# Performance work log

Hardware: AMD Instinct MI355X
Metric: run time of the kernel (lower is better)

Reference implementation:

```python
import jax, jax.numpy as jnp
import numpy as np

D_MODEL = 1024
N_HEADS = 16
D_HEAD = D_MODEL // N_HEADS


def setup_inputs() -> dict:
    key = jax.random.key(0)
    k_x, k_qkv, k_proj = jax.random.split(key, 3)
    x = jax.random.normal(k_x, (4, 2048, D_MODEL), dtype=jnp.float32)
    # nn.Linear(d_model, 3*d_model, bias=False): weight shape [3*d_model, d_model]
    scale = 1.0 / np.sqrt(D_MODEL)
    W_qkv = jax.random.uniform(k_qkv, (3 * D_MODEL, D_MODEL), dtype=jnp.float32, minval=-scale, maxval=scale)
    W_proj = jax.random.uniform(k_proj, (D_MODEL, D_MODEL), dtype=jnp.float32, minval=-scale, maxval=scale)
    return {"x": x, "W_qkv": W_qkv, "W_proj": W_proj}


def reference(x, W_qkv, W_proj):
    B, T, C = x.shape
    qkv = jnp.einsum('btc,fc->btf', x, W_qkv)  # [B,T,3C]
    q, k, v = jnp.split(qkv, 3, axis=-1)
    # [B,T,H,Dh] -> [B,H,T,Dh]
    q = q.reshape(B, T, N_HEADS, D_HEAD).transpose(0, 2, 1, 3)
    k = k.reshape(B, T, N_HEADS, D_HEAD).transpose(0, 2, 1, 3)
    v = v.reshape(B, T, N_HEADS, D_HEAD).transpose(0, 2, 1, 3)
    att = jnp.einsum('bhqd,bhkd->bhqk', q, k) / jnp.sqrt(jnp.float32(D_HEAD))
    att = jax.nn.softmax(att, axis=-1)
    y = jnp.einsum('bhqk,bhkd->bhqd', att, v)
    y = y.transpose(0, 2, 1, 3).reshape(B, T, C)
    return jnp.einsum('btc,oc->bto', y, W_proj)
```

## Files before the change

### kernel.cpp

```cpp
#include <hip/hip_runtime.h>
#include <stdint.h>
#include <stddef.h>

#define SEQ   2048
#define NH    16
#define DH    64
#define DM    1024
#define NTOK  8192

typedef unsigned short u16;
typedef unsigned int u32;
typedef short bf16x8 __attribute__((ext_vector_type(8)));
typedef float f32x4  __attribute__((ext_vector_type(4)));
typedef unsigned short u16x4 __attribute__((ext_vector_type(4)));
typedef unsigned short u16x8 __attribute__((ext_vector_type(8)));

#define QSCALE 0.18033688011112042f

#define WAIT_VM12 0x0F7C
#define WAIT_VM2  0x0F72
#define WAIT_VM0  0x0F70

__device__ __forceinline__ u16 f2bf(float f) {
  union { float f; unsigned u; } v; v.f = f;
  return (u16)((v.u + 0x7FFFu + ((v.u >> 16) & 1u)) >> 16);
}

__device__ __forceinline__ void gload_lds16(const void* g, void* l) {
  __builtin_amdgcn_global_load_lds(
      (const __attribute__((address_space(1))) void*)g,
      (__attribute__((address_space(3))) void*)l, 16, 0, 0);
}

__global__ __launch_bounds__(256) void cast_kernel(const float* __restrict__ src,
                                                   u16* __restrict__ dst, int n4) {
  int i = blockIdx.x * 256 + threadIdx.x;
  if (i < n4) {
    const float4 f = ((const float4*)src)[i];
    u16x4 o;
    o.x = f2bf(f.x); o.y = f2bf(f.y); o.z = f2bf(f.z); o.w = f2bf(f.w);
    ((u16x4*)dst)[i] = o;
  }
}

__global__ __launch_bounds__(256) void pack_b(const float* __restrict__ W,
                                              u16* __restrict__ Bp, int NS) {
  const int chunk = blockIdx.x * 256 + threadIdx.x;
  const int lane = chunk & 63, blk = chunk >> 6;
  const int c = blk / NS, s = blk % NS;
  const int n = s * 16 + (lane & 15);
  const int k0 = c * 32 + (lane >> 4) * 8;
  const float4 f0 = *(const float4*)&W[(size_t)n * DM + k0];
  const float4 f1 = *(const float4*)&W[(size_t)n * DM + k0 + 4];
  u16x8 o;
  o[0] = f2bf(f0.x); o[1] = f2bf(f0.y); o[2] = f2bf(f0.z); o[3] = f2bf(f0.w);
  o[4] = f2bf(f1.x); o[5] = f2bf(f1.y); o[6] = f2bf(f1.z); o[7] = f2bf(f1.w);
  *(u16x8*)&Bp[(size_t)chunk * 8] = o;
}

template <int EPI>
__global__ __launch_bounds__(256) void gemm_flat(
    const u16* __restrict__ A, const u16* __restrict__ Bp, int NS, int N_,
    u16* __restrict__ Qo, u16* __restrict__ Ko, u16* __restrict__ Vto,
    float* __restrict__ Co) {
  __shared__ __align__(16) u16 sA[2][128 * 64];
  const int tid = threadIdx.x;
  const int wave = tid >> 6, lane = tid & 63;
  const int l16 = lane & 15, quad = lane >> 4;
  const int sw = l16 & 7;
  const int wm = (wave >> 1) * 64, wn = (wave & 1) * 64;
  const int nbx = (int)gridDim.x;
  const int id = (int)(blockIdx.y * nbx + blockIdx.x);
  const int cpx = (int)(gridDim.x * gridDim.y) >> 3;
  const int wid = (id & 7) * cpx + (id >> 3);
  const int row0 = (wid / nbx) * 128, col0 = (wid % nbx) * 128;
  const int ck0 = ((quad ^ sw) << 3);
  const int ck1 = (((quad + 4) ^ sw) << 3);
  const int scol = (col0 + wn) >> 4;
  const u16* bpw = Bp + (size_t)lane * 8;

  f32x4 acc[4][4];
  for (int a = 0; a < 4; ++a)
    for (int b = 0; b < 4; ++b) acc[a][b] = (f32x4){0.f, 0.f, 0.f, 0.f};

  bf16x8 bfr[2][2][4];

  for (int j = 0; j < 4; ++j) {
    const int li = j * 256 + tid;
    const int r = li >> 3;
    const int cs = (((li & 7) ^ (r & 7)) << 3);
    gload_lds16(A + (size_t)(row0 + r) * DM + cs, (char*)sA[0] + li * 16);
  }
  for (int kk = 0; kk < 2; ++kk) {
    const u16* bb = bpw + ((size_t)kk * NS + scol) * 512;
    for (int i = 0; i < 4; ++i)
      bfr[0][kk][i] = *(const bf16x8*)(bb + i * 512);
  }

#pragma unroll 2
  for (int t = 0; t < 16; ++t) {
    const int cur = t & 1;
    const int tn = (t + 1) & 15;
    const int k1 = tn << 6;
    for (int j = 0; j < 4; ++j) {
      const int li = j * 256 + tid;
      const int r = li >> 3;
      const int cs = (((li & 7) ^ (r & 7)) << 3);
      gload_lds16(A + (size_t)(row0 + r) * DM + k1 + cs, (char*)sA[cur ^ 1] + li * 16);
    }
    for (int kk = 0; kk < 2; ++kk) {
      const u16* bb = bpw + ((size_t)(tn * 2 + kk) * NS + scol) * 512;
      for (int i = 0; i < 4; ++i)
        bfr[cur ^ 1][kk][i] = *(const bf16x8*)(bb + i * 512);
    }
    __builtin_amdgcn_s_waitcnt(WAIT_VM12);
    __builtin_amdgcn_s_barrier();
    const u16* sa = sA[cur];
    for (int kk = 0; kk < 2; ++kk) {
      const int cko = kk ? ck1 : ck0;
      bf16x8 af[4];
      for (int i = 0; i < 4; ++i)
        af[i] = *(const bf16x8*)&sa[(wm + i * 16 + l16) * 64 + cko];
      for (int mi = 0; mi < 4; ++mi)
        for (int ni = 0; ni < 4; ++ni)
          acc[mi][ni] = __builtin_amdgcn_mfma_f32_16x16x32_bf16(
              af[mi], bfr[cur][kk][ni], acc[mi][ni], 0, 0, 0);
    }
    __builtin_amdgcn_s_barrier();
  }
  __builtin_amdgcn_s_waitcnt(WAIT_VM0);

  if (EPI == 0) {
    const int which = col0 >> 10;
    for (int mi = 0; mi < 4; ++mi)
      for (int ni = 0; ni < 4; ++ni) {
        const int rowb = row0 + wm + mi * 16 + quad * 4;
        const int col = col0 + wn + ni * 16 + l16;
        const int b = rowb >> 11, t = rowb & (SEQ - 1);
        const int c = col & (DM - 1);
        const int h = c >> 6, d = c & 63;
        const size_t bh = (size_t)b * NH + h;
        if (which == 2) {
          u16x4 pk;
          pk.x = f2bf(acc[mi][ni][0]); pk.y = f2bf(acc[mi][ni][1]);
          pk.z = f2bf(acc[mi][ni][2]); pk.w = f2bf(acc[mi][ni][3]);
          *(u16x4*)&Vto[(bh * DH + d) * SEQ + t] = pk;
        } else {
          for (int r = 0; r < 4; ++r) {
            const float v = acc[mi][ni][r];
            if (which == 0) Qo[(bh * SEQ + t + r) * DH + d] = f2bf(v * QSCALE);
            else            Ko[(bh * SEQ + t + r) * DH + d] = f2bf(v);
          }
        }
      }
  } else {
    for (int mi = 0; mi < 4; ++mi)
      for (int ni = 0; ni < 4; ++ni)
        for (int r = 0; r < 4; ++r) {
          const int row = row0 + wm + mi * 16 + quad * 4 + r;
          const int col = col0 + wn + ni * 16 + l16;
          Co[(size_t)row * N_ + col] = acc[mi][ni][r];
        }
  }
}

#define PSTRIDE 72
__global__ __launch_bounds__(512) void flash_attn(
    const u16* __restrict__ Q, const u16* __restrict__ Kk,
    const u16* __restrict__ Vt, u16* __restrict__ Y) {
  __shared__ __align__(16) u16 sK[2][64 * 64];
  __shared__ __align__(16) u16 sV[2][64 * 64];
  __shared__ __align__(16) u16 sP[8 * 32 * PSTRIDE];
  const int tid = threadIdx.x, wave = tid >> 6, lane = tid & 63;
  const int l16 = lane & 15, quad = lane >> 4;
  const int sw = l16 & 7;
  const int ck0 = ((quad ^ sw) << 3);
  const int ck1 = (((quad + 4) ^ sw) << 3);
  const int rloc = tid >> 3;
  const int cs = (((tid & 7) ^ (rloc & 7)) << 3);
  const int id = (int)(blockIdx.y * 8 + blockIdx.x);
  const int wid = (id & 7) * 64 + (id >> 3);
  const int bh = wid >> 3;
  const int q0 = (wid & 7) * 256 + wave * 32;
  const size_t qkBase = (size_t)bh * SEQ * DH;
  const size_t vtBase = (size_t)bh * DH * SEQ;

  bf16x8 qf[2][2];
  for (int ms = 0; ms < 2; ++ms) {
    const u16* qrow = Q + qkBase + (size_t)(q0 + ms * 16 + l16) * DH;
    qf[ms][0] = *(const bf16x8*)(qrow + quad * 8);
    qf[ms][1] = *(const bf16x8*)(qrow + 32 + quad * 8);
  }

  bf16x8 onesf;
  for (int i = 0; i < 8; ++i) onesf[i] = (short)0x3F80;

  f32x4 o[2][4];
  f32x4 osum[2];
  for (int a = 0; a < 2; ++a) {
    osum[a] = (f32x4){0.f, 0.f, 0.f, 0.f};
    for (int b = 0; b < 4; ++b) o[a][b] = (f32x4){0.f, 0.f, 0.f, 0.f};
  }

  u16* myP = sP + wave * 32 * PSTRIDE;

  gload_lds16(Kk + qkBase + (size_t)rloc * DH + cs, (char*)sK[0] + tid * 16);
  gload_lds16(Vt + vtBase + (size_t)rloc * SEQ + cs, (char*)sV[0] + tid * 16);
  for (int t = 0; t < 32; ++t) {
    const int cur = t & 1;
    const int kt1 = ((t + 1) & 31) * 64;
    gload_lds16(Kk + qkBase + (size_t)(kt1 + rloc) * DH + cs, (char*)sK[cur ^ 1] + tid * 16);
    gload_lds16(Vt + vtBase + (size_t)rloc * SEQ + kt1 + cs, (char*)sV[cur ^ 1] + tid * 16);
    __builtin_amdgcn_s_waitcnt(WAIT_VM2);
    __builtin_amdgcn_s_barrier();
    const u16* sk = sK[cur];
    const u16* sv = sV[cur];

    for (int nt = 0; nt < 4; ++nt) {
      bf16x8 kf0 = *(const bf16x8*)&sk[(nt * 16 + l16) * 64 + ck0];
      bf16x8 kf1 = *(const bf16x8*)&sk[(nt * 16 + l16) * 64 + ck1];
      for (int ms = 0; ms < 2; ++ms) {
        f32x4 st = (f32x4){0.f, 0.f, 0.f, 0.f};
        __builtin_amdgcn_s_setprio(1);
        st = __builtin_amdgcn_mfma_f32_16x16x32_bf16(kf0, qf[ms][0], st, 0, 0, 0);
        st = __builtin_amdgcn_mfma_f32_16x16x32_bf16(kf1, qf[ms][1], st, 0, 0, 0);
        __builtin_amdgcn_s_setprio(0);
        const u32 u0 = __builtin_bit_cast(u32, __builtin_amdgcn_exp2f(st[0]));
        const u32 u1 = __builtin_bit_cast(u32, __builtin_amdgcn_exp2f(st[1]));
        const u32 u2 = __builtin_bit_cast(u32, __builtin_amdgcn_exp2f(st[2]));
        const u32 u3 = __builtin_bit_cast(u32, __builtin_amdgcn_exp2f(st[3]));
        uint2 pk;
        pk.x = __builtin_amdgcn_perm(u1, u0, 0x07060302u);
        pk.y = __builtin_amdgcn_perm(u3, u2, 0x07060302u);
        *(uint2*)&myP[(ms * 16 + l16) * PSTRIDE + nt * 16 + quad * 4] = pk;
      }
    }

    bf16x8 pf[2][2];
    for (int ms = 0; ms < 2; ++ms) {
      pf[ms][0] = *(const bf16x8*)&myP[(ms * 16 + l16) * PSTRIDE + quad * 8];
      pf[ms][1] = *(const bf16x8*)&myP[(ms * 16 + l16) * PSTRIDE + 32 + quad * 8];
    }
    __builtin_amdgcn_s_setprio(1);
    for (int ms = 0; ms < 2; ++ms) {
      osum[ms] = __builtin_amdgcn_mfma_f32_16x16x32_bf16(pf[ms][0], onesf, osum[ms], 0, 0, 0);
      osum[ms] = __builtin_amdgcn_mfma_f32_16x16x32_bf16(pf[ms][1], onesf, osum[ms], 0, 0, 0);
    }
    for (int ds = 0; ds < 4; ++ds) {
      bf16x8 vf0 = *(const bf16x8*)&sv[(ds * 16 + l16) * 64 + ck0];
      bf16x8 vf1 = *(const bf16x8*)&sv[(ds * 16 + l16) * 64 + ck1];
      for (int ms = 0; ms < 2; ++ms) {
        o[ms][ds] = __builtin_amdgcn_mfma_f32_16x16x32_bf16(pf[ms][0], vf0, o[ms][ds], 0, 0, 0);
        o[ms][ds] = __builtin_amdgcn_mfma_f32_16x16x32_bf16(pf[ms][1], vf1, o[ms][ds], 0, 0, 0);
      }
    }
    __builtin_amdgcn_s_setprio(0);
    __builtin_amdgcn_s_barrier();
  }
  __builtin_amdgcn_s_waitcnt(WAIT_VM0);

  float rl[2][4];
  for (int ms = 0; ms < 2; ++ms)
    for (int r = 0; r < 4; ++r)
      rl[ms][r] = __frcp_rn(osum[ms][r]);

  const int b = bh >> 4, h = bh & (NH - 1);
  for (int ms = 0; ms < 2; ++ms)
    for (int ds = 0; ds < 4; ++ds)
      for (int r = 0; r < 4; ++r) {
        const int t = q0 + ms * 16 + quad * 4 + r;
        const int d = ds * 16 + l16;
        Y[((size_t)(b * SEQ + t)) * DM + h * DH + d] = f2bf(o[ms][ds][r] * rl[ms][r]);
      }
}

extern "C" void kernel_launch(void* const* d_in, const int* in_sizes, int n_in,
                              void* d_out, int out_size, void* d_ws, size_t ws_size,
                              hipStream_t stream) {
  const float* x     = (const float*)d_in[0];
  const float* Wqkv  = (const float*)d_in[1];
  const float* Wproj = (const float*)d_in[2];
  float* out = (float*)d_out;

  u16* xb     = (u16*)d_ws;
  u16* bpQkv  = xb + (size_t)NTOK * DM;
  u16* bpProj = bpQkv + (size_t)3 * DM * DM;
  u16* Qb  = bpProj + (size_t)DM * DM;
  u16* Kb  = Qb + (size_t)NTOK * DM;
  u16* Vtb = Kb + (size_t)NTOK * DM;
  u16* Yb  = Vtb + (size_t)NTOK * DM;

  {
    int n4 = NTOK * DM / 4;
    cast_kernel<<<(n4 + 255) / 256, 256, 0, stream>>>(x, xb, n4);
    pack_b<<<3 * DM * DM / 8 / 256, 256, 0, stream>>>(Wqkv, bpQkv, 3 * DM / 16);
    pack_b<<<DM * DM / 8 / 256, 256, 0, stream>>>(Wproj, bpProj, DM / 16);
  }

  gemm_flat<0><<<dim3(3 * DM / 128, NTOK / 128), 256, 0, stream>>>(
      xb, bpQkv, 3 * DM / 16, 3 * DM, Qb, Kb, Vtb, nullptr);

  flash_attn<<<dim3(SEQ / 256, 4 * NH), 512, 0, stream>>>(Qb, Kb, Vtb, Yb);

  gemm_flat<1><<<dim3(DM / 128, NTOK / 128), 256, 0, stream>>>(
      Yb, bpProj, DM / 16, DM, nullptr, nullptr, nullptr, out);
}
```

Baseline: 258.2 us.

## Keep softmax P in registers and permute V loads to match accumulator layout

The attention kernel no longer writes exp'd scores to a shared-memory P buffer and reads them back as MFMA operands. The S accumulator fragments are packed directly into registers and used as the A operand of the PV and row-sum MFMAs. To make this valid, the V fragments are gathered with two 4-element LDS reads in a permuted k order that matches the register layout. This removes the LDS round trip and its shared-memory footprint, and adds a launch-bounds occupancy hint, in exchange for more, smaller LDS reads of V.

```diff
diff --git a/kernel.cpp b/kernel.cpp
--- a/kernel.cpp
+++ b/kernel.cpp
@@ -11,9 +11,11 @@
 typedef unsigned short u16;
 typedef unsigned int u32;
 typedef short bf16x8 __attribute__((ext_vector_type(8)));
+typedef short bf16x4 __attribute__((ext_vector_type(4)));
 typedef float f32x4  __attribute__((ext_vector_type(4)));
 typedef unsigned short u16x4 __attribute__((ext_vector_type(4)));
 typedef unsigned short u16x8 __attribute__((ext_vector_type(8)));
+typedef unsigned int u32x4 __attribute__((ext_vector_type(4)));
 
 #define QSCALE 0.18033688011112042f
 
@@ -30,6 +32,13 @@
   __builtin_amdgcn_global_load_lds(
       (const __attribute__((address_space(1))) void*)g,
       (__attribute__((address_space(3))) void*)l, 16, 0, 0);
+}
+
+__device__ __forceinline__ bf16x8 cat44(bf16x4 a, bf16x4 b) {
+  bf16x8 r;
+  r[0] = a[0]; r[1] = a[1]; r[2] = a[2]; r[3] = a[3];
+  r[4] = b[0]; r[5] = b[1]; r[6] = b[2]; r[7] = b[3];
+  return r;
 }
 
 __global__ __launch_bounds__(256) void cast_kernel(const float* __restrict__ src,
@@ -164,13 +173,11 @@
   }
 }
 
-#define PSTRIDE 72
-__global__ __launch_bounds__(512) void flash_attn(
+__global__ __launch_bounds__(512, 6) void flash_attn(
     const u16* __restrict__ Q, const u16* __restrict__ Kk,
     const u16* __restrict__ Vt, u16* __restrict__ Y) {
   __shared__ __align__(16) u16 sK[2][64 * 64];
   __shared__ __align__(16) u16 sV[2][64 * 64];
-  __shared__ __align__(16) u16 sP[8 * 32 * PSTRIDE];
   const int tid = threadIdx.x, wave = tid >> 6, lane = tid & 63;
   const int l16 = lane & 15, quad = lane >> 4;
   const int sw = l16 & 7;
@@ -185,6 +192,12 @@
   const size_t qkBase = (size_t)bh * SEQ * DH;
   const size_t vtBase = (size_t)bh * DH * SEQ;
 
+  const int q2 = quad >> 1, q1o = (quad & 1) << 2;
+  const int vA0 = (((q2 + 0) ^ sw) << 3) + q1o;
+  const int vB0 = (((q2 + 2) ^ sw) << 3) + q1o;
+  const int vA1 = (((q2 + 4) ^ sw) << 3) + q1o;
+  const int vB1 = (((q2 + 6) ^ sw) << 3) + q1o;
+
   bf16x8 qf[2][2];
   for (int ms = 0; ms < 2; ++ms) {
     const u16* qrow = Q + qkBase + (size_t)(q0 + ms * 16 + l16) * DH;
@@ -201,8 +214,6 @@
     osum[a] = (f32x4){0.f, 0.f, 0.f, 0.f};
     for (int b = 0; b < 4; ++b) o[a][b] = (f32x4){0.f, 0.f, 0.f, 0.f};
   }
-
-  u16* myP = sP + wave * 32 * PSTRIDE;
 
   gload_lds16(Kk + qkBase + (size_t)rloc * DH + cs, (char*)sK[0] + tid * 16);
   gload_lds16(Vt + vtBase + (size_t)rloc * SEQ + cs, (char*)sV[0] + tid * 16);
@@ -216,9 +227,12 @@
     const u16* sk = sK[cur];
     const u16* sv = sV[cur];
 
+    u32x4 pw[2][2];
+#pragma unroll
     for (int nt = 0; nt < 4; ++nt) {
-      bf16x8 kf0 = *(const bf16x8*)&sk[(nt * 16 + l16) * 64 + ck0];
-      bf16x8 kf1 = *(const bf16x8*)&sk[(nt * 16 + l16) * 64 + ck1];
+      const bf16x8 kf0 = *(const bf16x8*)&sk[(nt * 16 + l16) * 64 + ck0];
+      const bf16x8 kf1 = *(const bf16x8*)&sk[(nt * 16 + l16) * 64 + ck1];
+#pragma unroll
       for (int ms = 0; ms < 2; ++ms) {
         f32x4 st = (f32x4){0.f, 0.f, 0.f, 0.f};
         __builtin_amdgcn_s_setprio(1);
@@ -229,29 +243,33 @@
         const u32 u1 = __builtin_bit_cast(u32, __builtin_amdgcn_exp2f(st[1]));
         const u32 u2 = __builtin_bit_cast(u32, __builtin_amdgcn_exp2f(st[2]));
         const u32 u3 = __builtin_bit_cast(u32, __builtin_amdgcn_exp2f(st[3]));
-        uint2 pk;
-        pk.x = __builtin_amdgcn_perm(u1, u0, 0x07060302u);
-        pk.y = __builtin_amdgcn_perm(u3, u2, 0x07060302u);
-        *(uint2*)&myP[(ms * 16 + l16) * PSTRIDE + nt * 16 + quad * 4] = pk;
+        pw[ms][nt >> 1][(nt & 1) * 2]     = __builtin_amdgcn_perm(u1, u0, 0x07060302u);
+        pw[ms][nt >> 1][(nt & 1) * 2 + 1] = __builtin_amdgcn_perm(u3, u2, 0x07060302u);
       }
     }
 
-    bf16x8 pf[2][2];
+    __builtin_amdgcn_s_setprio(1);
+#pragma unroll
     for (int ms = 0; ms < 2; ++ms) {
-      pf[ms][0] = *(const bf16x8*)&myP[(ms * 16 + l16) * PSTRIDE + quad * 8];
-      pf[ms][1] = *(const bf16x8*)&myP[(ms * 16 + l16) * PSTRIDE + 32 + quad * 8];
-    }
-    __builtin_amdgcn_s_setprio(1);
-    for (int ms = 0; ms < 2; ++ms) {
-      osum[ms] = __builtin_amdgcn_mfma_f32_16x16x32_bf16(pf[ms][0], onesf, osum[ms], 0, 0, 0);
-      osum[ms] = __builtin_amdgcn_mfma_f32_16x16x32_bf16(pf[ms][1], onesf, osum[ms], 0, 0, 0);
-    }
+      osum[ms] = __builtin_amdgcn_mfma_f32_16x16x32_bf16(
+          __builtin_bit_cast(bf16x8, pw[ms][0]), onesf, osum[ms], 0, 0, 0);
+      osum[ms] = __builtin_amdgcn_mfma_f32_16x16x32_bf16(
+          __builtin_bit_cast(bf16x8, pw[ms][1]), onesf, osum[ms], 0, 0, 0);
+    }
+
+#pragma unroll
     for (int ds = 0; ds < 4; ++ds) {
-      bf16x8 vf0 = *(const bf16x8*)&sv[(ds * 16 + l16) * 64 + ck0];
-      bf16x8 vf1 = *(const bf16x8*)&sv[(ds * 16 + l16) * 64 + ck1];
+      const int rb = (ds * 16 + l16) * 64;
+      const bf16x8 vf0 = cat44(*(const bf16x4*)&sv[rb + vA0],
+                               *(const bf16x4*)&sv[rb + vB0]);
+      const bf16x8 vf1 = cat44(*(const bf16x4*)&sv[rb + vA1],
+                               *(const bf16x4*)&sv[rb + vB1]);
+#pragma unroll
       for (int ms = 0; ms < 2; ++ms) {
-        o[ms][ds] = __builtin_amdgcn_mfma_f32_16x16x32_bf16(pf[ms][0], vf0, o[ms][ds], 0, 0, 0);
-        o[ms][ds] = __builtin_amdgcn_mfma_f32_16x16x32_bf16(pf[ms][1], vf1, o[ms][ds], 0, 0, 0);
+        o[ms][ds] = __builtin_amdgcn_mfma_f32_16x16x32_bf16(
+            __builtin_bit_cast(bf16x8, pw[ms][0]), vf0, o[ms][ds], 0, 0, 0);
+        o[ms][ds] = __builtin_amdgcn_mfma_f32_16x16x32_bf16(
+            __builtin_bit_cast(bf16x8, pw[ms][1]), vf1, o[ms][ds], 0, 0, 0);
       }
     }
     __builtin_amdgcn_s_setprio(0);
```

After: 440.8 us. 70.7% more time.
